# Kernel optimization log

Measured on AMD Instinct MI355X. Metric: run time of the kernel, lower is better.

## Reference

```python
import jax, jax.numpy as jnp
import numpy as np

MIN_LEVEL, MAX_LEVEL = 3, 7
IMG = 1024
BASE_SIZE = 4
RATIOS = (0.5, 1.0, 2.0)
LO, HI = 0.4, 0.5  # min_iou_thresh, max_iou_thresh


def _make_anchors():
    outs, sizes = [], []
    for lvl in range(MIN_LEVEL, MAX_LEVEL + 1):
        stride = 2 ** lvl
        size = BASE_SIZE * stride
        anch = []
        for r in RATIOS:
            h = size * np.sqrt(r)
            w = size / np.sqrt(r)
            anch.append([-w / 2, -h / 2, w / 2, h / 2])
        anch = np.array(anch, np.float32)                      # [A,4]
        n = IMG // stride
        c = (np.arange(n, dtype=np.float32) + 0.5) * stride
        sx, sy = np.meshgrid(c, c)
        shifts = np.stack([sx, sy, sx, sy], -1).reshape(-1, 1, 4)
        lvl_anch = (shifts + anch[None]).reshape(-1, 4)        # [n*n*A,4]
        outs.append(lvl_anch)
        sizes.append(lvl_anch.shape[0])
    return np.concatenate(outs, 0).astype(np.float32), sizes

ANCHORS_NP, LEVEL_SIZES = _make_anchors()   # total 65472 anchors, sizes [49152,12288,3072,768,192]


def _pair_iou(anch, g):
    # anch [N,4], g [G,4] -> IoU [N,G]
    x1 = jnp.maximum(anch[:, None, 0], g[None, :, 0])
    y1 = jnp.maximum(anch[:, None, 1], g[None, :, 1])
    x2 = jnp.minimum(anch[:, None, 2], g[None, :, 2])
    y2 = jnp.minimum(anch[:, None, 3], g[None, :, 3])
    inter = jnp.clip(x2 - x1, 0.0) * jnp.clip(y2 - y1, 0.0)
    aa = (anch[:, 2] - anch[:, 0]) * (anch[:, 3] - anch[:, 1])
    ag = (g[:, 2] - g[:, 0]) * (g[:, 3] - g[:, 1])
    return inter / (aa[:, None] + ag[None, :] - inter + 1e-9)


def _bbox_transform(anch, gt):
    # anchor/gt boxes [...,4] (x1,y1,x2,y2) -> (dx,dy,dw,dh)
    aw = anch[..., 2] - anch[..., 0]
    ah = anch[..., 3] - anch[..., 1]
    ax = anch[..., 0] + 0.5 * aw
    ay = anch[..., 1] + 0.5 * ah
    gw = gt[..., 2] - gt[..., 0]
    gh = gt[..., 3] - gt[..., 1]
    gx = gt[..., 0] + 0.5 * gw
    gy = gt[..., 1] + 0.5 * gh
    return jnp.stack([(gx - ax) / aw, (gy - ay) / ah,
                      jnp.log(gw / aw), jnp.log(gh / ah)], -1)


def setup_inputs() -> dict:
    key = jax.random.key(0)
    k1, k2, k3, k4 = jax.random.split(key, 4)
    B, G = 16, 32
    cx = jax.random.uniform(k1, (B, G), minval=64.0, maxval=960.0)
    cy = jax.random.uniform(k2, (B, G), minval=64.0, maxval=960.0)
    hw = jax.random.uniform(k3, (B, G), minval=8.0, maxval=150.0)
    hh = jax.random.uniform(k4, (B, G), minval=8.0, maxval=150.0)
    bb_coord = jnp.stack([jnp.clip(cx - hw, 0, IMG), jnp.clip(cy - hh, 0, IMG),
                          jnp.clip(cx + hw, 0, IMG), jnp.clip(cy + hh, 0, IMG)], -1).astype(jnp.float32)
    bird_ids = jax.random.randint(jax.random.fold_in(key, 1), (B, G), 1, 81, dtype=jnp.int32)
    anchors = jnp.asarray(ANCHORS_NP)
    return {"bb_coord": bb_coord, "bird_ids": bird_ids, "anchors": anchors}


def reference(bb_coord, bird_ids, anchors):
    # bb_coord [B,G,4] float, bird_ids [B,G] int, anchors [N_total,4] float
    B, G = bird_ids.shape
    offs = np.cumsum([0] + LEVEL_SIZES)
    # IoUs per level: [B,N_l,G]
    per = []
    for li in range(len(LEVEL_SIZES)):
        anch = anchors[offs[li]:offs[li + 1]]
        ov = jax.vmap(lambda g: _pair_iou(anch, g))(bb_coord)
        per.append((anch, ov))
    # best level per GT (argmax of per-level best anchor IoU)
    gt_max = jnp.stack([ov.max(axis=1) for _, ov in per], 0)     # [L,B,G]
    gt_max_level = jnp.argmax(gt_max, axis=0)                    # [B,G]
    bidx = jnp.arange(B)[:, None]
    labels_all, regs_all = [], []
    for li, (anch, ov) in enumerate(per):
        N = anch.shape[0]
        max_ov = ov.max(axis=2)                                  # [B,N]
        arg = jnp.argmax(ov, axis=2)                             # [B,N]
        assigned_box = bb_coord[bidx, arg]                       # [B,N,4]
        assigned_id = bird_ids[bidx, arg]                        # [B,N]
        gt_arg = jnp.argmax(ov, axis=1)                          # [B,G] best anchor per GT
        sel = gt_max_level == li                                 # GTs forced onto this level
        sidx = jnp.where(sel, gt_arg, N)                         # scatter to pad slot N when unselected
        ab = jnp.concatenate([assigned_box, jnp.zeros((B, 1, 4), bb_coord.dtype)], 1)
        ab = ab.at[bidx, sidx].set(bb_coord)[:, :N]
        ai = jnp.concatenate([assigned_id, jnp.zeros((B, 1), bird_ids.dtype)], 1)
        ai = ai.at[bidx, sidx].set(bird_ids)[:, :N]
        pos = jnp.concatenate([max_ov >= HI, jnp.zeros((B, 1), bool)], 1)
        pos = pos.at[bidx, sidx].set(True)[:, :N]
        ign = (max_ov >= LO) & (max_ov < HI)
        label = jnp.where(pos, ai, jnp.where(ign, -1, 0)).astype(jnp.int32)
        reg = jnp.where(pos[..., None], _bbox_transform(anch[None], ab), 0.0)
        labels_all.append(label)
        regs_all.append(reg)
    return jnp.concatenate(labels_all, 1), jnp.concatenate(regs_all, 1)
```

## Files before the change

kernel.cpp:

```cpp
#include <hip/hip_runtime.h>

#pragma clang fp contract(off)

#define A_TOTAL 65472
#define NB 16
#define NG 32
#define NLVL 5


__global__ __launch_bounds__(256) void fused_kernel(
    const float* __restrict__ bb,
    const int* __restrict__ ids,
    const float* __restrict__ anchors,
    unsigned long long* __restrict__ part,
    float* __restrict__ out)
{
    const int wid  = threadIdx.x >> 6;
    const int lane = threadIdx.x & 63;
    const int b = blockIdx.x >> 7;
    const int w = ((blockIdx.x & 127) << 2) + wid;
    const int start = w << 7;
    const bool full = (w != 511);
    const int lvl = (w < 384) ? 0 : (w < 480) ? 1 : (w < 504) ? 2 : (w < 510) ? 3 : 4;

    __shared__ float4 sbb[NG];
    __shared__ float  sag[NG];
    __shared__ int    sid[NG];
    if (threadIdx.x < NG) {
        float4 q = ((const float4*)bb)[b * NG + threadIdx.x];
        sbb[threadIdx.x] = q;
        sag[threadIdx.x] = (q.z - q.x) * (q.w - q.y);
        sid[threadIdx.x] = ids[b * NG + threadIdx.x];
    }
    __syncthreads();

    float4 an[2];
    float  aa[2];
    an[0] = ((const float4*)anchors)[start + lane];
    aa[0] = (an[0].z - an[0].x) * (an[0].w - an[0].y);
    if (full) {
        an[1] = ((const float4*)anchors)[start + 64 + lane];
        aa[1] = (an[1].z - an[1].x) * (an[1].w - an[1].y);
    } else {
        an[1] = an[0]; aa[1] = aa[0];
    }

    float abest[2] = {-1.0f, -1.0f};
    int   agid[2]  = {0, 0};
    unsigned long long red = 0ull;

    for (int g = 0; g < NG; ++g) {
        const float4 q  = sbb[g];
        const float  ag = sag[g];
        unsigned long long key = 0ull;
#pragma unroll
        for (int k = 0; k < 2; ++k) {
            if (k == 1 && !full) continue;
            const unsigned int n = (unsigned int)(start + (k << 6) + lane);
            float x1 = fmaxf(an[k].x, q.x);
            float y1 = fmaxf(an[k].y, q.y);
            float x2 = fminf(an[k].z, q.z);
            float y2 = fminf(an[k].w, q.w);
            float ww = fmaxf(x2 - x1, 0.0f);
            float hh = fmaxf(y2 - y1, 0.0f);
            float inter = ww * hh;
            float denom = aa[k] + ag - inter + 1e-9f;
            float v = inter / denom;
            unsigned long long kk =
                ((unsigned long long)__float_as_uint(v) << 32) |
                (unsigned long long)(~n);
            if (kk > key) key = kk;
            if (v > abest[k]) { abest[k] = v; agid[k] = g; }
        }
#pragma unroll
        for (int s = 1; s < 64; s <<= 1) {
            unsigned long long o = __shfl_xor(key, s, 64);
            if (o > key) key = o;
        }
        if (lane == g) red = key;
    }
    if (lane < NG) {
        atomicMax(&part[(b * NG + lane) * NLVL + lvl], red);
    }

#pragma unroll
    for (int k = 0; k < 2; ++k) {
        if (k == 1 && !full) continue;
        const int n = start + (k << 6) + lane;
        float label;
        float4 rg;
        if (abest[k] >= 0.5f) {
            const float4 gtb = sbb[agid[k]];
            label = (float)sid[agid[k]];
            float aw = an[k].z - an[k].x;
            float ah = an[k].w - an[k].y;
            float ax = an[k].x + 0.5f * aw;
            float ay = an[k].y + 0.5f * ah;
            float gw = gtb.z - gtb.x;
            float gh = gtb.w - gtb.y;
            float gx = gtb.x + 0.5f * gw;
            float gy = gtb.y + 0.5f * gh;
            rg = make_float4((gx - ax) / aw, (gy - ay) / ah, logf(gw / aw), logf(gh / ah));
        } else {
            label = (abest[k] >= 0.4f) ? -1.0f : 0.0f;
            rg = make_float4(0.0f, 0.0f, 0.0f, 0.0f);
        }
        out[b * A_TOTAL + n] = label;
        ((float4*)(out + NB * A_TOTAL))[b * A_TOTAL + n] = rg;
    }
}

__global__ __launch_bounds__(512) void tail_kernel(
    const float* __restrict__ bb,
    const int* __restrict__ ids,
    const float* __restrict__ anchors,
    unsigned long long* __restrict__ part,
    float* __restrict__ out)
{
    const int t = threadIdx.x;
    __shared__ int sfor[NB * NG];

    unsigned long long k0 = atomicMax(&part[t * NLVL + 0], 0ull);
    unsigned int bestf = (unsigned int)(k0 >> 32);
    unsigned long long bestk = k0;
#pragma unroll
    for (int l = 1; l < NLVL; ++l) {
        unsigned long long kl = atomicMax(&part[t * NLVL + l], 0ull);
        unsigned int f = (unsigned int)(kl >> 32);
        if (f > bestf) { bestf = f; bestk = kl; }
    }
    const int n = (int)(~(unsigned int)(bestk & 0xFFFFFFFFull));
    sfor[t] = n;
    __syncthreads();

    const int b = t >> 5;
    const int g = t & 31;
    bool shadowed = false;
    for (int g2 = g + 1; g2 < NG; ++g2)
        if (sfor[(b << 5) | g2] == n) shadowed = true;

    if (!shadowed) {
        const float4 gtb = ((const float4*)bb)[t];
        const float4 an  = ((const float4*)anchors)[n];
        float aw = an.z - an.x;
        float ah = an.w - an.y;
        float ax = an.x + 0.5f * aw;
        float ay = an.y + 0.5f * ah;
        float gw = gtb.z - gtb.x;
        float gh = gtb.w - gtb.y;
        float gx = gtb.x + 0.5f * gw;
        float gy = gtb.y + 0.5f * gh;
        out[b * A_TOTAL + n] = (float)ids[t];
        ((float4*)(out + NB * A_TOTAL))[b * A_TOTAL + n] =
            make_float4((gx - ax) / aw, (gy - ay) / ah, logf(gw / aw), logf(gh / ah));
    }
}

extern "C" void kernel_launch(void* const* d_in, const int* in_sizes, int n_in,
                              void* d_out, int out_size, void* d_ws, size_t ws_size,
                              hipStream_t stream) {
    const float* bb      = (const float*)d_in[0];
    const int*   ids     = (const int*)d_in[1];
    const float* anchors = (const float*)d_in[2];
    float* out = (float*)d_out;

    unsigned long long* part = (unsigned long long*)d_ws;

    hipMemsetAsync(part, 0, NB * NG * NLVL * sizeof(unsigned long long), stream);
    hipLaunchKernelGGL(fused_kernel, dim3(NB * 128), dim3(256), 0, stream,
                       bb, ids, anchors, part, out);
    hipLaunchKernelGGL(tail_kernel, dim3(1), dim3(512), 0, stream,
                       bb, ids, anchors, part, out);
}
```

Before: 118.5 us.

## Fold tail into last-block epilogue, widen per-lane anchors, pair GTs in reductions

```diff
diff --git a/kernel.cpp b/kernel.cpp
--- a/kernel.cpp
+++ b/kernel.cpp
@@ -5,23 +5,22 @@
 #define A_TOTAL 65472
 #define NB 16
 #define NG 32
-#define NLVL 5
 
 
 __global__ __launch_bounds__(256) void fused_kernel(
     const float* __restrict__ bb,
     const int* __restrict__ ids,
     const float* __restrict__ anchors,
-    unsigned long long* __restrict__ part,
+    unsigned long long* __restrict__ part2,
+    unsigned int* __restrict__ counter,
     float* __restrict__ out)
 {
     const int wid  = threadIdx.x >> 6;
     const int lane = threadIdx.x & 63;
-    const int b = blockIdx.x >> 7;
-    const int w = ((blockIdx.x & 127) << 2) + wid;
-    const int start = w << 7;
-    const bool full = (w != 511);
-    const int lvl = (w < 384) ? 0 : (w < 480) ? 1 : (w < 504) ? 2 : (w < 510) ? 3 : 4;
+    const int b = blockIdx.x >> 6;
+    const int r = ((blockIdx.x & 63) << 2) + wid;
+    const int start = r << 8;
+    const bool full = (r != 255);
 
     __shared__ float4 sbb[NG];
     __shared__ float  sag[NG];
@@ -34,58 +33,81 @@
     }
     __syncthreads();
 
-    float4 an[2];
-    float  aa[2];
-    an[0] = ((const float4*)anchors)[start + lane];
-    aa[0] = (an[0].z - an[0].x) * (an[0].w - an[0].y);
-    if (full) {
-        an[1] = ((const float4*)anchors)[start + 64 + lane];
-        aa[1] = (an[1].z - an[1].x) * (an[1].w - an[1].y);
-    } else {
-        an[1] = an[0]; aa[1] = aa[0];
+    float4 an[4];
+    float  aa[4];
+#pragma unroll
+    for (int k = 0; k < 4; ++k) {
+        if (k == 3 && !full) { an[3] = an[0]; aa[3] = aa[0]; continue; }
+        an[k] = ((const float4*)anchors)[start + (k << 6) + lane];
+        aa[k] = (an[k].z - an[k].x) * (an[k].w - an[k].y);
     }
 
-    float abest[2] = {-1.0f, -1.0f};
-    int   agid[2]  = {0, 0};
+    float abest[4] = {-1.0f, -1.0f, -1.0f, -1.0f};
+    int   agid[4]  = {0, 0, 0, 0};
     unsigned long long red = 0ull;
 
-    for (int g = 0; g < NG; ++g) {
-        const float4 q  = sbb[g];
-        const float  ag = sag[g];
-        unsigned long long key = 0ull;
+    for (int j = 0; j < 16; ++j) {
+        const int g0 = j << 1;
+        const int g1 = g0 + 1;
+        const float4 q0 = sbb[g0]; const float ag0 = sag[g0];
+        const float4 q1 = sbb[g1]; const float ag1 = sag[g1];
+
+        float v0 = -1.0f, v1 = -1.0f;
+        unsigned int n0 = 0u, n1 = 0u;
 #pragma unroll
-        for (int k = 0; k < 2; ++k) {
-            if (k == 1 && !full) continue;
+        for (int k = 0; k < 4; ++k) {
+            if (k == 3 && !full) continue;
             const unsigned int n = (unsigned int)(start + (k << 6) + lane);
-            float x1 = fmaxf(an[k].x, q.x);
-            float y1 = fmaxf(an[k].y, q.y);
-            float x2 = fminf(an[k].z, q.z);
-            float y2 = fminf(an[k].w, q.w);
-            float ww = fmaxf(x2 - x1, 0.0f);
-            float hh = fmaxf(y2 - y1, 0.0f);
-            float inter = ww * hh;
-            float denom = aa[k] + ag - inter + 1e-9f;
-            float v = inter / denom;
-            unsigned long long kk =
-                ((unsigned long long)__float_as_uint(v) << 32) |
-                (unsigned long long)(~n);
-            if (kk > key) key = kk;
-            if (v > abest[k]) { abest[k] = v; agid[k] = g; }
+            {
+                float x1 = fmaxf(an[k].x, q0.x);
+                float y1 = fmaxf(an[k].y, q0.y);
+                float x2 = fminf(an[k].z, q0.z);
+                float y2 = fminf(an[k].w, q0.w);
+                float ww = fmaxf(x2 - x1, 0.0f);
+                float hh = fmaxf(y2 - y1, 0.0f);
+                float inter = ww * hh;
+                float denom = aa[k] + ag0 - inter + 1e-9f;
+                float v = inter / denom;
+                if (v > v0) { v0 = v; n0 = n; }
+                if (v > abest[k]) { abest[k] = v; agid[k] = g0; }
+            }
+            {
+                float x1 = fmaxf(an[k].x, q1.x);
+                float y1 = fmaxf(an[k].y, q1.y);
+                float x2 = fminf(an[k].z, q1.z);
+                float y2 = fminf(an[k].w, q1.w);
+                float ww = fmaxf(x2 - x1, 0.0f);
+                float hh = fmaxf(y2 - y1, 0.0f);
+                float inter = ww * hh;
+                float denom = aa[k] + ag1 - inter + 1e-9f;
+                float v = inter / denom;
+                if (v > v1) { v1 = v; n1 = n; }
+                if (v > abest[k]) { abest[k] = v; agid[k] = g1; }
+            }
         }
+        unsigned long long k0 =
+            ((unsigned long long)__float_as_uint(v0) << 32) | (unsigned long long)(~n0);
+        unsigned long long k1 =
+            ((unsigned long long)__float_as_uint(v1) << 32) | (unsigned long long)(~n1);
+        unsigned long long x = (lane < 32) ? k0 : k1;
+        unsigned long long y = __shfl_xor((lane < 32) ? k1 : k0, 32, 64);
+        if (y > x) x = y;
 #pragma unroll
-        for (int s = 1; s < 64; s <<= 1) {
-            unsigned long long o = __shfl_xor(key, s, 64);
-            if (o > key) key = o;
+        for (int s = 1; s < 32; s <<= 1) {
+            unsigned long long o = __shfl_xor(x, s, 64);
+            if (o > x) x = o;
         }
-        if (lane == g) red = key;
+        unsigned long long y2 = __shfl_xor(x, 32, 64);
+        if (lane == g0) red = x;
+        if (lane == g1) red = y2;
     }
     if (lane < NG) {
-        atomicMax(&part[(b * NG + lane) * NLVL + lvl], red);
+        atomicMax(&part2[b * NG + lane], red);
     }
 
 #pragma unroll
-    for (int k = 0; k < 2; ++k) {
-        if (k == 1 && !full) continue;
+    for (int k = 0; k < 4; ++k) {
+        if (k == 3 && !full) continue;
         const int n = start + (k << 6) + lane;
         float label;
         float4 rg;
@@ -108,51 +130,44 @@
         out[b * A_TOTAL + n] = label;
         ((float4*)(out + NB * A_TOTAL))[b * A_TOTAL + n] = rg;
     }
-}
 
-__global__ __launch_bounds__(512) void tail_kernel(
-    const float* __restrict__ bb,
-    const int* __restrict__ ids,
-    const float* __restrict__ anchors,
-    unsigned long long* __restrict__ part,
-    float* __restrict__ out)
-{
-    const int t = threadIdx.x;
+    __shared__ int sdone;
+    __syncthreads();
+    if (threadIdx.x == 0) {
+        __threadfence();
+        sdone = (atomicAdd(counter, 1u) == (unsigned int)(gridDim.x - 1)) ? 1 : 0;
+    }
+    __syncthreads();
+    if (!sdone) return;
+
     __shared__ int sfor[NB * NG];
-
-    unsigned long long k0 = atomicMax(&part[t * NLVL + 0], 0ull);
-    unsigned int bestf = (unsigned int)(k0 >> 32);
-    unsigned long long bestk = k0;
-#pragma unroll
-    for (int l = 1; l < NLVL; ++l) {
-        unsigned long long kl = atomicMax(&part[t * NLVL + l], 0ull);
-        unsigned int f = (unsigned int)(kl >> 32);
-        if (f > bestf) { bestf = f; bestk = kl; }
+    for (int t = threadIdx.x; t < NB * NG; t += 256) {
+        unsigned long long kk = atomicMax(&part2[t], 0ull);
+        sfor[t] = (int)(~(unsigned int)(kk & 0xFFFFFFFFull));
     }
-    const int n = (int)(~(unsigned int)(bestk & 0xFFFFFFFFull));
-    sfor[t] = n;
     __syncthreads();
-
-    const int b = t >> 5;
-    const int g = t & 31;
-    bool shadowed = false;
-    for (int g2 = g + 1; g2 < NG; ++g2)
-        if (sfor[(b << 5) | g2] == n) shadowed = true;
-
-    if (!shadowed) {
-        const float4 gtb = ((const float4*)bb)[t];
-        const float4 an  = ((const float4*)anchors)[n];
-        float aw = an.z - an.x;
-        float ah = an.w - an.y;
-        float ax = an.x + 0.5f * aw;
-        float ay = an.y + 0.5f * ah;
-        float gw = gtb.z - gtb.x;
-        float gh = gtb.w - gtb.y;
-        float gx = gtb.x + 0.5f * gw;
-        float gy = gtb.y + 0.5f * gh;
-        out[b * A_TOTAL + n] = (float)ids[t];
-        ((float4*)(out + NB * A_TOTAL))[b * A_TOTAL + n] =
-            make_float4((gx - ax) / aw, (gy - ay) / ah, logf(gw / aw), logf(gh / ah));
+    for (int t = threadIdx.x; t < NB * NG; t += 256) {
+        const int bi = t >> 5;
+        const int g  = t & 31;
+        const int n  = sfor[t];
+        bool shadowed = false;
+        for (int g2 = g + 1; g2 < NG; ++g2)
+            if (sfor[(bi << 5) | g2] == n) shadowed = true;
+        if (!shadowed) {
+            const float4 gtb = ((const float4*)bb)[t];
+            const float4 a   = ((const float4*)anchors)[n];
+            float aw = a.z - a.x;
+            float ah = a.w - a.y;
+            float ax = a.x + 0.5f * aw;
+            float ay = a.y + 0.5f * ah;
+            float gw = gtb.z - gtb.x;
+            float gh = gtb.w - gtb.y;
+            float gx = gtb.x + 0.5f * gw;
+            float gy = gtb.y + 0.5f * gh;
+            out[bi * A_TOTAL + n] = (float)ids[t];
+            ((float4*)(out + NB * A_TOTAL))[bi * A_TOTAL + n] =
+                make_float4((gx - ax) / aw, (gy - ay) / ah, logf(gw / aw), logf(gh / ah));
+        }
     }
 }
 
@@ -164,11 +179,10 @@
     const float* anchors = (const float*)d_in[2];
     float* out = (float*)d_out;
 
-    unsigned long long* part = (unsigned long long*)d_ws;
+    unsigned long long* part2 = (unsigned long long*)d_ws;
+    unsigned int* counter = (unsigned int*)((char*)d_ws + NB * NG * 8);
 
-    hipMemsetAsync(part, 0, NB * NG * NLVL * sizeof(unsigned long long), stream);
-    hipLaunchKernelGGL(fused_kernel, dim3(NB * 128), dim3(256), 0, stream,
-                       bb, ids, anchors, part, out);
-    hipLaunchKernelGGL(tail_kernel, dim3(1), dim3(512), 0, stream,
-                       bb, ids, anchors, part, out);
+    hipMemsetAsync(d_ws, 0, NB * NG * 8 + 64, stream);
+    hipLaunchKernelGGL(fused_kernel, dim3(NB * 64), dim3(256), 0, stream,
+                       bb, ids, anchors, part2, counter, out);
 }
```

After: 121.7 us. 1.03x slower.
